# Kernel tuning notes

Hardware: AMD Instinct MI355X
Metric: run time of the kernel (lower is better)

## Reference

```python
import jax, jax.numpy as jnp
import numpy as np

Q_HEADS, KV_HEADS, DIMS = 16, 4, 1024
HEAD_DIM = DIMS // Q_HEADS          # 64
GROUPS = Q_HEADS // KV_HEADS        # 4
ROPE_BASE = 10000.0


def rope(x):
    # x: (..., s, d) -- standard interleaved rotary embedding, base 10000
    s, d = x.shape[-2], x.shape[-1]
    inv_freq = 1.0 / (ROPE_BASE ** (jnp.arange(0, d, 2, dtype=jnp.float32) / d))
    ang = jnp.arange(s, dtype=jnp.float32)[:, None] * inv_freq[None, :]  # (s, d/2)
    cos, sin = jnp.cos(ang), jnp.sin(ang)
    x1, x2 = x[..., 0::2], x[..., 1::2]
    out = jnp.stack([x1 * cos - x2 * sin, x1 * sin + x2 * cos], axis=-1)
    return out.reshape(x.shape).astype(x.dtype)


def setup_inputs() -> dict:
    key = jax.random.key(0)
    k1, k2, k3, k4, k5, k6 = jax.random.split(key, 6)
    B, S, E = 4, 2048, 1024
    q = jax.random.normal(k1, (B, S, E), dtype=jnp.float32)
    kv = jax.random.normal(k2, (B, S, E), dtype=jnp.float32)
    sc = 1.0 / np.sqrt(E)
    Wq = jax.random.normal(k3, (E, Q_HEADS, HEAD_DIM), dtype=jnp.float32) * sc
    Wk = jax.random.normal(k4, (E, KV_HEADS, HEAD_DIM), dtype=jnp.float32) * sc
    Wv = jax.random.normal(k5, (E, KV_HEADS, HEAD_DIM), dtype=jnp.float32) * sc
    Wo = jax.random.normal(k6, (HEAD_DIM, E), dtype=jnp.float32) / np.sqrt(HEAD_DIM)
    return {"q": q, "kv": kv, "Wq": Wq, "Wk": Wk, "Wv": Wv, "Wo": Wo}


def reference(q, kv, Wq, Wk, Wv, Wo):
    B, S, E = q.shape
    qh = jnp.einsum('bse,ehd->bshd', q, Wq)    # (B,S,Q_HEADS,hd)
    kh = jnp.einsum('bse,ehd->bshd', kv, Wk)   # (B,S,KV_HEADS,hd)
    vh = jnp.einsum('bse,ehd->bshd', kv, Wv)
    # rearrange '... s (h g) d -> ... g h s d' with g=GROUPS (h = KV_HEADS outer)
    qh = qh.reshape(B, S, KV_HEADS, GROUPS, HEAD_DIM).transpose(0, 3, 2, 1, 4)  # (B,g,h,S,d)
    kh = kh.transpose(0, 2, 1, 3)  # (B,h,S,d)
    vh = vh.transpose(0, 2, 1, 3)  # (B,h,S,d)
    qh = rope(qh)
    kh = rope(kh)
    # NOTE: sums over group axis g (faithful to original einsum)
    scores = jnp.einsum('bghsd,bhad->bhsa', qh, kh)
    attn = jax.nn.softmax(scores / (HEAD_DIM ** 0.5), axis=-1)
    out = jnp.einsum('bhsa,bhad->bhsd', attn, vh)  # (B,h,S,d)
    out = out.mean(axis=1)                          # mean over kv heads -> (B,S,d)
    return out @ Wo                                 # (B,S,E)
```

## Files before the change

kernel.cpp:

```cpp
#include <hip/hip_runtime.h>
#include <math.h>

#define SS 2048
#define EE 1024

using bf16x8 = __attribute__((ext_vector_type(8))) short;
using f32x4  = __attribute__((ext_vector_type(4))) float;

__device__ inline short f2bf(float x) {
    unsigned u = __builtin_bit_cast(unsigned, x);
    return (short)((u + 0x7fffu + ((u >> 16) & 1u)) >> 16);
}

__global__ __launch_bounds__(256) void prep_weights(const float* __restrict__ Wq,
                                                    const float* __restrict__ Wk,
                                                    const float* __restrict__ Wv,
                                                    const float* __restrict__ Wo,
                                                    short* __restrict__ Wall,
                                                    short* __restrict__ Wo4) {
    int idx = blockIdx.x * 256 + threadIdx.x;
    int c = idx >> 10, e = idx & 1023;
    int h = c >> 6, d = c & 63;
    const float* p = Wq + (size_t)e * 1024 + h * 256 + d;
    Wall[(size_t)c * 1024 + e] = f2bf(0.18033688011112042f * (p[0] + p[64] + p[128] + p[192]));
    Wall[(size_t)(256 + c) * 1024 + e] = f2bf(Wk[(size_t)e * 256 + c]);
    Wall[(size_t)(512 + c) * 1024 + e] = f2bf(Wv[(size_t)e * 256 + c]);
    Wo4[(size_t)e * 256 + c] = f2bf(0.25f * Wo[(size_t)d * 1024 + e]);
}

__global__ __launch_bounds__(256) void proj_kernel(const float* __restrict__ q,
                                                   const float* __restrict__ kv,
                                                   const short* __restrict__ Wall,
                                                   short* __restrict__ Qb,
                                                   short* __restrict__ Kb,
                                                   short* __restrict__ Vb) {
    __shared__ short As[128][72];
    __shared__ short Bs[64][72];
    int tid = threadIdx.x;
    int wave = tid >> 6, lane = tid & 63, quad = lane >> 4, c16 = lane & 15;
    int wm = wave >> 1, wn = wave & 1;
    int m0 = blockIdx.x * 128, n0 = blockIdx.y * 64;
    const float* A = (n0 < 256) ? q : kv;

    f32x4 acc[4][2];
    #pragma unroll
    for (int i = 0; i < 4; i++)
        #pragma unroll
        for (int j = 0; j < 2; j++) acc[i][j] = (f32x4){0.f, 0.f, 0.f, 0.f};

    for (int k0 = 0; k0 < 1024; k0 += 64) {
        #pragma unroll
        for (int i = 0; i < 8; i++) {
            int id = i * 256 + tid, r = id >> 4, ch = id & 15;
            float4 v = *(const float4*)&A[(size_t)(m0 + r) * 1024 + k0 + ch * 4];
            short4 s4;
            s4.x = f2bf(v.x); s4.y = f2bf(v.y); s4.z = f2bf(v.z); s4.w = f2bf(v.w);
            *(short4*)&As[r][ch * 4] = s4;
        }
        #pragma unroll
        for (int i = 0; i < 2; i++) {
            int id = i * 256 + tid, r = id >> 3, ch = id & 7;
            *(int4*)&Bs[r][ch * 8] =
                *(const int4*)&Wall[(size_t)(n0 + r) * 1024 + k0 + ch * 8];
        }
        __syncthreads();
        #pragma unroll
        for (int ks = 0; ks < 64; ks += 32) {
            bf16x8 af[4], bfr[2];
            #pragma unroll
            for (int mt = 0; mt < 4; mt++)
                af[mt] = *(const bf16x8*)&As[wm * 64 + mt * 16 + c16][ks + quad * 8];
            #pragma unroll
            for (int nt = 0; nt < 2; nt++)
                bfr[nt] = *(const bf16x8*)&Bs[wn * 32 + nt * 16 + c16][ks + quad * 8];
            #pragma unroll
            for (int mt = 0; mt < 4; mt++)
                #pragma unroll
                for (int nt = 0; nt < 2; nt++)
                    acc[mt][nt] = __builtin_amdgcn_mfma_f32_16x16x32_bf16(
                        af[mt], bfr[nt], acc[mt][nt], 0, 0, 0);
        }
        __syncthreads();
    }
    #pragma unroll
    for (int mt = 0; mt < 4; mt++) {
        #pragma unroll
        for (int nt = 0; nt < 2; nt++) {
            int col = n0 + wn * 32 + nt * 16 + c16;
            int rowb = m0 + wm * 64 + mt * 16 + quad * 4;
            f32x4 v = acc[mt][nt];
            short* dst = (col < 256) ? (Qb + col)
                       : (col < 512) ? (Kb + col - 256)
                                     : (Vb + col - 512);
            if (col < 512) {
                int d = col & 63, ii = d >> 1;
                float freq = __expf(-(float)ii * (9.210340371976184f / 32.0f));
                float sgn = (lane & 1) ? 1.0f : -1.0f;
                #pragma unroll
                for (int r = 0; r < 4; r++) {
                    int row = rowb + r;
                    float ang = (float)(row & (SS - 1)) * freq;
                    float sn, cs;
                    sincosf(ang, &sn, &cs);
                    float other = __shfl_xor(v[r], 1);
                    dst[(size_t)row * 256] = f2bf(v[r] * cs + sgn * sn * other);
                }
            } else {
                #pragma unroll
                for (int r = 0; r < 4; r++)
                    dst[(size_t)(rowb + r) * 256] = f2bf(v[r]);
            }
        }
    }
}

__global__ __launch_bounds__(256) void transpose_v(const short* __restrict__ Vb,
                                                   short* __restrict__ Vt) {
    __shared__ short T[64][72];
    int t = threadIdx.x;
    int s0 = blockIdx.x * 64, h = blockIdx.y, b = blockIdx.z;
    #pragma unroll
    for (int i = 0; i < 2; i++) {
        int id = i * 256 + t, sl = id >> 3, ch = id & 7;
        *(int4*)&T[sl][ch * 8] =
            *(const int4*)&Vb[((size_t)(b * SS + s0 + sl)) * 256 + h * 64 + ch * 8];
    }
    __syncthreads();
    #pragma unroll
    for (int i = 0; i < 2; i++) {
        int id = i * 256 + t, d = id >> 3, ch = id & 7;
        bf16x8 o;
        #pragma unroll
        for (int j = 0; j < 8; j++) o[j] = T[ch * 8 + j][d];
        *(bf16x8*)&Vt[((size_t)((b * 4 + h) * 64 + d)) * SS + s0 + ch * 8] = o;
    }
}

__global__ __launch_bounds__(256) void attn_kernel(const short* __restrict__ Qb,
                                                   const short* __restrict__ Kb,
                                                   const short* __restrict__ Vt,
                                                   float* __restrict__ Opart,
                                                   float* __restrict__ Lpart) {
    __shared__ short Qs[64][72], Ks[64][72], Vs[64][72];
    __shared__ short Ps[4][16][72];
    int tid = threadIdx.x;
    int wave = tid >> 6, lane = tid & 63, quad = lane >> 4, c16 = lane & 15;
    int qt = blockIdx.x, bh = blockIdx.y, kc = blockIdx.z;
    int q0 = qt * 64;
    size_t qkbase = (size_t)(bh >> 2) * SS * 256 + (bh & 3) * 64;
    size_t vtbase = (size_t)(bh * 64) * SS;
    size_t pbase  = (size_t)(kc * 16 + bh) * SS;

    #pragma unroll
    for (int i = 0; i < 2; i++) {
        int id = i * 256 + tid, r = id >> 3, ch = id & 7;
        *(int4*)&Qs[r][ch * 8] = *(const int4*)&Qb[qkbase + (size_t)(q0 + r) * 256 + ch * 8];
    }
    __syncthreads();
    bf16x8 aq0 = *(const bf16x8*)&Qs[wave * 16 + c16][quad * 8];
    bf16x8 aq1 = *(const bf16x8*)&Qs[wave * 16 + c16][32 + quad * 8];

    float lsum[4] = {0.f, 0.f, 0.f, 0.f};
    f32x4 o[4];
    #pragma unroll
    for (int dt = 0; dt < 4; dt++) o[dt] = (f32x4){0.f, 0.f, 0.f, 0.f};

    for (int kt = 0; kt < 16; kt++) {
        int a0 = kc * 1024 + kt * 64;
        __syncthreads();
        #pragma unroll
        for (int i = 0; i < 2; i++) {
            int id = i * 256 + tid, r = id >> 3, ch = id & 7;
            *(int4*)&Ks[r][ch * 8] =
                *(const int4*)&Kb[qkbase + (size_t)(a0 + r) * 256 + ch * 8];
            *(int4*)&Vs[r][ch * 8] =
                *(const int4*)&Vt[vtbase + (size_t)r * SS + a0 + ch * 8];
        }
        __syncthreads();
        f32x4 sv[4];
        #pragma unroll
        for (int nt = 0; nt < 4; nt++) sv[nt] = (f32x4){0.f, 0.f, 0.f, 0.f};
        #pragma unroll
        for (int nt = 0; nt < 4; nt++) {
            bf16x8 bk0 = *(const bf16x8*)&Ks[nt * 16 + c16][quad * 8];
            bf16x8 bk1 = *(const bf16x8*)&Ks[nt * 16 + c16][32 + quad * 8];
            sv[nt] = __builtin_amdgcn_mfma_f32_16x16x32_bf16(aq0, bk0, sv[nt], 0, 0, 0);
            sv[nt] = __builtin_amdgcn_mfma_f32_16x16x32_bf16(aq1, bk1, sv[nt], 0, 0, 0);
        }
        #pragma unroll
        for (int nt = 0; nt < 4; nt++)
            #pragma unroll
            for (int r = 0; r < 4; r++) sv[nt][r] = __builtin_exp2f(sv[nt][r]);
        #pragma unroll
        for (int r = 0; r < 4; r++)
            lsum[r] += (sv[0][r] + sv[1][r]) + (sv[2][r] + sv[3][r]);
        #pragma unroll
        for (int nt = 0; nt < 4; nt++)
            #pragma unroll
            for (int r = 0; r < 4; r++)
                Ps[wave][quad * 4 + r][nt * 16 + c16] = f2bf(sv[nt][r]);
        #pragma unroll
        for (int ks = 0; ks < 64; ks += 32) {
            bf16x8 ap = *(const bf16x8*)&Ps[wave][c16][ks + quad * 8];
            #pragma unroll
            for (int dt = 0; dt < 4; dt++) {
                bf16x8 bv = *(const bf16x8*)&Vs[dt * 16 + c16][ks + quad * 8];
                o[dt] = __builtin_amdgcn_mfma_f32_16x16x32_bf16(ap, bv, o[dt], 0, 0, 0);
            }
        }
    }
    #pragma unroll
    for (int off = 1; off < 16; off <<= 1)
        #pragma unroll
        for (int r = 0; r < 4; r++) lsum[r] += __shfl_xor(lsum[r], off);
    #pragma unroll
    for (int dt = 0; dt < 4; dt++)
        #pragma unroll
        for (int r = 0; r < 4; r++) {
            int row = q0 + wave * 16 + quad * 4 + r;
            Opart[(pbase + row) * 64 + dt * 16 + c16] = o[dt][r];
        }
    if (c16 == 0)
        #pragma unroll
        for (int r = 0; r < 4; r++)
            Lpart[pbase + q0 + wave * 16 + quad * 4 + r] = lsum[r];
}

__global__ __launch_bounds__(256) void combine_kernel(const float* __restrict__ Opart,
                                                      const float* __restrict__ Lpart,
                                                      float* __restrict__ Ob) {
    int idx = blockIdx.x * 256 + threadIdx.x;
    int d = idx & 63, h = (idx >> 6) & 3, s = (idx >> 8) & 2047, b = idx >> 19;
    int bh = b * 4 + h;
    size_t p0 = ((size_t)bh * SS + s) * 64 + d;
    size_t p1 = ((size_t)(16 + bh) * SS + s) * 64 + d;
    float o = Opart[p0] + Opart[p1];
    float l = Lpart[(size_t)bh * SS + s] + Lpart[(size_t)(16 + bh) * SS + s];
    Ob[((size_t)(b * SS + s)) * 256 + h * 64 + d] = o / l;
}

__global__ __launch_bounds__(256) void outproj_kernel(const float* __restrict__ Ob,
                                                      const short* __restrict__ Wo4,
                                                      float* __restrict__ out) {
    __shared__ short As[128][72];
    __shared__ short Bs[128][72];
    int tid = threadIdx.x;
    int wave = tid >> 6, lane = tid & 63, quad = lane >> 4, c16 = lane & 15;
    int wm = wave >> 1, wn = wave & 1;
    int m0 = blockIdx.x * 128, n0 = blockIdx.y * 128;

    f32x4 acc[4][4];
    #pragma unroll
    for (int i = 0; i < 4; i++)
        #pragma unroll
        for (int j = 0; j < 4; j++) acc[i][j] = (f32x4){0.f, 0.f, 0.f, 0.f};

    for (int k0 = 0; k0 < 256; k0 += 64) {
        #pragma unroll
        for (int i = 0; i < 8; i++) {
            int id = i * 256 + tid, r = id >> 4, ch = id & 15;
            float4 v = *(const float4*)&Ob[(size_t)(m0 + r) * 256 + k0 + ch * 4];
            short4 s4;
            s4.x = f2bf(v.x); s4.y = f2bf(v.y); s4.z = f2bf(v.z); s4.w = f2bf(v.w);
            *(short4*)&As[r][ch * 4] = s4;
        }
        #pragma unroll
        for (int i = 0; i < 4; i++) {
            int id = i * 256 + tid, r = id >> 3, ch = id & 7;
            *(int4*)&Bs[r][ch * 8] =
                *(const int4*)&Wo4[(size_t)(n0 + r) * 256 + k0 + ch * 8];
        }
        __syncthreads();
        #pragma unroll
        for (int ks = 0; ks < 64; ks += 32) {
            bf16x8 af[4], bfr[4];
            #pragma unroll
            for (int mt = 0; mt < 4; mt++)
                af[mt] = *(const bf16x8*)&As[wm * 64 + mt * 16 + c16][ks + quad * 8];
            #pragma unroll
            for (int nt = 0; nt < 4; nt++)
                bfr[nt] = *(const bf16x8*)&Bs[wn * 64 + nt * 16 + c16][ks + quad * 8];
            #pragma unroll
            for (int mt = 0; mt < 4; mt++)
                #pragma unroll
                for (int nt = 0; nt < 4; nt++)
                    acc[mt][nt] = __builtin_amdgcn_mfma_f32_16x16x32_bf16(
                        af[mt], bfr[nt], acc[mt][nt], 0, 0, 0);
        }
        __syncthreads();
    }
    #pragma unroll
    for (int mt = 0; mt < 4; mt++)
        #pragma unroll
        for (int nt = 0; nt < 4; nt++) {
            int col = n0 + wn * 64 + nt * 16 + c16;
            int rowb = m0 + wm * 64 + mt * 16 + quad * 4;
            #pragma unroll
            for (int r = 0; r < 4; r++)
                out[(size_t)(rowb + r) * 1024 + col] = acc[mt][nt][r];
        }
}

extern "C" void kernel_launch(void* const* d_in, const int* in_sizes, int n_in,
                              void* d_out, int out_size, void* d_ws, size_t ws_size,
                              hipStream_t stream) {
    const float* q  = (const float*)d_in[0];
    const float* kv = (const float*)d_in[1];
    const float* Wq = (const float*)d_in[2];
    const float* Wk = (const float*)d_in[3];
    const float* Wv = (const float*)d_in[4];
    const float* Wo = (const float*)d_in[5];
    float* out = (float*)d_out;

    short* Qb    = (short*)d_ws;
    short* Kb    = Qb + 2097152;
    short* Vb    = Kb + 2097152;
    short* Vt    = Vb + 2097152;
    short* Wall  = Vt + 2097152;
    short* Wo4   = Wall + 786432;
    float* Ob    = (float*)(Wo4 + 262144);
    float* Opart = Ob + 2097152;
    float* Lpart = Opart + 4194304;

    prep_weights<<<1024, 256, 0, stream>>>(Wq, Wk, Wv, Wo, Wall, Wo4);

    proj_kernel<<<dim3(64, 12), 256, 0, stream>>>(q, kv, Wall, Qb, Kb, Vb);

    transpose_v<<<dim3(32, 4, 4), 256, 0, stream>>>(Vb, Vt);

    attn_kernel<<<dim3(32, 16, 2), 256, 0, stream>>>(Qb, Kb, Vt, Opart, Lpart);

    combine_kernel<<<8192, 256, 0, stream>>>(Opart, Lpart, Ob);

    outproj_kernel<<<dim3(64, 8), 256, 0, stream>>>(Ob, Wo4, out);
}
```

Measured before the change: 212.4 us.

## Fuse V transpose into projection and split-K combine into output projection

The projection epilogue now writes V directly in transposed layout, so the separate transpose kernel is removed. The combine of the two split-K partial results is folded into the output projection's A-tile load, which removes the Ob round trip and one launch. RoPE cos/sin values are precomputed into a table in prep_weights instead of calling sincosf per element. bf16 conversion switches to cheaper round-half-up packing with perm, which changes the rounding behaviour slightly.

```diff
diff --git a/kernel.cpp b/kernel.cpp
--- a/kernel.cpp
+++ b/kernel.cpp
@@ -10,6 +10,14 @@
 __device__ inline short f2bf(float x) {
     unsigned u = __builtin_bit_cast(unsigned, x);
     return (short)((u + 0x7fffu + ((u >> 16) & 1u)) >> 16);
+}
+__device__ inline short f2bf_r(float x) {
+    return (short)((__builtin_bit_cast(unsigned, x) + 0x8000u) >> 16);
+}
+__device__ inline unsigned pk_bf16(float a, float b) {
+    unsigned ua = __builtin_bit_cast(unsigned, a) + 0x8000u;
+    unsigned ub = __builtin_bit_cast(unsigned, b) + 0x8000u;
+    return __builtin_amdgcn_perm(ub, ua, 0x07060302u);
 }
 
 __global__ __launch_bounds__(256) void prep_weights(const float* __restrict__ Wq,
@@ -17,7 +25,8 @@
                                                     const float* __restrict__ Wv,
                                                     const float* __restrict__ Wo,
                                                     short* __restrict__ Wall,
-                                                    short* __restrict__ Wo4) {
+                                                    short* __restrict__ Wo4,
+                                                    float2* __restrict__ RT) {
     int idx = blockIdx.x * 256 + threadIdx.x;
     int c = idx >> 10, e = idx & 1023;
     int h = c >> 6, d = c & 63;
@@ -26,14 +35,22 @@
     Wall[(size_t)(256 + c) * 1024 + e] = f2bf(Wk[(size_t)e * 256 + c]);
     Wall[(size_t)(512 + c) * 1024 + e] = f2bf(Wv[(size_t)e * 256 + c]);
     Wo4[(size_t)e * 256 + c] = f2bf(0.25f * Wo[(size_t)d * 1024 + e]);
+    if (idx < 65536) {
+        int s = idx >> 5, ii = idx & 31;
+        float freq = __expf(-(float)ii * (9.210340371976184f / 32.0f));
+        float sn, cs;
+        sincosf((float)s * freq, &sn, &cs);
+        RT[idx] = (float2){cs, sn};
+    }
 }
 
 __global__ __launch_bounds__(256) void proj_kernel(const float* __restrict__ q,
                                                    const float* __restrict__ kv,
                                                    const short* __restrict__ Wall,
+                                                   const float2* __restrict__ RT,
                                                    short* __restrict__ Qb,
                                                    short* __restrict__ Kb,
-                                                   short* __restrict__ Vb) {
+                                                   short* __restrict__ Vt) {
     __shared__ short As[128][72];
     __shared__ short Bs[64][72];
     int tid = threadIdx.x;
@@ -53,9 +70,10 @@
         for (int i = 0; i < 8; i++) {
             int id = i * 256 + tid, r = id >> 4, ch = id & 15;
             float4 v = *(const float4*)&A[(size_t)(m0 + r) * 1024 + k0 + ch * 4];
-            short4 s4;
-            s4.x = f2bf(v.x); s4.y = f2bf(v.y); s4.z = f2bf(v.z); s4.w = f2bf(v.w);
-            *(short4*)&As[r][ch * 4] = s4;
+            uint2 u;
+            u.x = pk_bf16(v.x, v.y);
+            u.y = pk_bf16(v.z, v.w);
+            *(uint2*)&As[r][ch * 4] = u;
         }
         #pragma unroll
         for (int i = 0; i < 2; i++) {
@@ -89,50 +107,26 @@
             int col = n0 + wn * 32 + nt * 16 + c16;
             int rowb = m0 + wm * 64 + mt * 16 + quad * 4;
             f32x4 v = acc[mt][nt];
-            short* dst = (col < 256) ? (Qb + col)
-                       : (col < 512) ? (Kb + col - 256)
-                                     : (Vb + col - 512);
             if (col < 512) {
-                int d = col & 63, ii = d >> 1;
-                float freq = __expf(-(float)ii * (9.210340371976184f / 32.0f));
+                short* dst = (col < 256) ? (Qb + col) : (Kb + col - 256);
+                int ii = (col & 63) >> 1;
                 float sgn = (lane & 1) ? 1.0f : -1.0f;
                 #pragma unroll
                 for (int r = 0; r < 4; r++) {
                     int row = rowb + r;
-                    float ang = (float)(row & (SS - 1)) * freq;
-                    float sn, cs;
-                    sincosf(ang, &sn, &cs);
+                    float2 cs = RT[(row & (SS - 1)) * 32 + ii];
                     float other = __shfl_xor(v[r], 1);
-                    dst[(size_t)row * 256] = f2bf(v[r] * cs + sgn * sn * other);
+                    dst[(size_t)row * 256] = f2bf_r(v[r] * cs.x + sgn * cs.y * other);
                 }
             } else {
-                #pragma unroll
-                for (int r = 0; r < 4; r++)
-                    dst[(size_t)(rowb + r) * 256] = f2bf(v[r]);
+                int c = col - 512;
+                int b = rowb >> 11, s0 = rowb & (SS - 1);
+                uint2 u;
+                u.x = pk_bf16(v[0], v[1]);
+                u.y = pk_bf16(v[2], v[3]);
+                *(uint2*)&Vt[((size_t)(b * 256 + c)) * SS + s0] = u;
             }
         }
-    }
-}
-
-__global__ __launch_bounds__(256) void transpose_v(const short* __restrict__ Vb,
-                                                   short* __restrict__ Vt) {
-    __shared__ short T[64][72];
-    int t = threadIdx.x;
-    int s0 = blockIdx.x * 64, h = blockIdx.y, b = blockIdx.z;
-    #pragma unroll
-    for (int i = 0; i < 2; i++) {
-        int id = i * 256 + t, sl = id >> 3, ch = id & 7;
-        *(int4*)&T[sl][ch * 8] =
-            *(const int4*)&Vb[((size_t)(b * SS + s0 + sl)) * 256 + h * 64 + ch * 8];
-    }
-    __syncthreads();
-    #pragma unroll
-    for (int i = 0; i < 2; i++) {
-        int id = i * 256 + t, d = id >> 3, ch = id & 7;
-        bf16x8 o;
-        #pragma unroll
-        for (int j = 0; j < 8; j++) o[j] = T[ch * 8 + j][d];
-        *(bf16x8*)&Vt[((size_t)((b * 4 + h) * 64 + d)) * SS + s0 + ch * 8] = o;
     }
 }
 
@@ -198,7 +192,7 @@
         for (int nt = 0; nt < 4; nt++)
             #pragma unroll
             for (int r = 0; r < 4; r++)
-                Ps[wave][quad * 4 + r][nt * 16 + c16] = f2bf(sv[nt][r]);
+                Ps[wave][quad * 4 + r][nt * 16 + c16] = f2bf_r(sv[nt][r]);
         #pragma unroll
         for (int ks = 0; ks < 64; ks += 32) {
             bf16x8 ap = *(const bf16x8*)&Ps[wave][c16][ks + quad * 8];
@@ -226,20 +220,8 @@
             Lpart[pbase + q0 + wave * 16 + quad * 4 + r] = lsum[r];
 }
 
-__global__ __launch_bounds__(256) void combine_kernel(const float* __restrict__ Opart,
-                                                      const float* __restrict__ Lpart,
-                                                      float* __restrict__ Ob) {
-    int idx = blockIdx.x * 256 + threadIdx.x;
-    int d = idx & 63, h = (idx >> 6) & 3, s = (idx >> 8) & 2047, b = idx >> 19;
-    int bh = b * 4 + h;
-    size_t p0 = ((size_t)bh * SS + s) * 64 + d;
-    size_t p1 = ((size_t)(16 + bh) * SS + s) * 64 + d;
-    float o = Opart[p0] + Opart[p1];
-    float l = Lpart[(size_t)bh * SS + s] + Lpart[(size_t)(16 + bh) * SS + s];
-    Ob[((size_t)(b * SS + s)) * 256 + h * 64 + d] = o / l;
-}
-
-__global__ __launch_bounds__(256) void outproj_kernel(const float* __restrict__ Ob,
+__global__ __launch_bounds__(256) void outproj_kernel(const float* __restrict__ Op,
+                                                      const float* __restrict__ Lp,
                                                       const short* __restrict__ Wo4,
                                                       float* __restrict__ out) {
     __shared__ short As[128][72];
@@ -256,13 +238,21 @@
         for (int j = 0; j < 4; j++) acc[i][j] = (f32x4){0.f, 0.f, 0.f, 0.f};
 
     for (int k0 = 0; k0 < 256; k0 += 64) {
+        int h = k0 >> 6;
         #pragma unroll
         for (int i = 0; i < 8; i++) {
             int id = i * 256 + tid, r = id >> 4, ch = id & 15;
-            float4 v = *(const float4*)&Ob[(size_t)(m0 + r) * 256 + k0 + ch * 4];
-            short4 s4;
-            s4.x = f2bf(v.x); s4.y = f2bf(v.y); s4.z = f2bf(v.z); s4.w = f2bf(v.w);
-            *(short4*)&As[r][ch * 4] = s4;
+            int row = m0 + r, b = row >> 11, s = row & (SS - 1);
+            int bh = b * 4 + h;
+            size_t pidx = ((size_t)bh * SS + s) * 64 + ch * 4;
+            float4 a = *(const float4*)&Op[pidx];
+            float4 c = *(const float4*)&Op[pidx + (size_t)16 * SS * 64];
+            float l = Lp[(size_t)bh * SS + s] + Lp[(size_t)(16 + bh) * SS + s];
+            float rl = __builtin_amdgcn_rcpf(l);
+            uint2 u;
+            u.x = pk_bf16((a.x + c.x) * rl, (a.y + c.y) * rl);
+            u.y = pk_bf16((a.z + c.z) * rl, (a.w + c.w) * rl);
+            *(uint2*)&As[r][ch * 4] = u;
         }
         #pragma unroll
         for (int i = 0; i < 4; i++) {
@@ -314,23 +304,18 @@
 
     short* Qb    = (short*)d_ws;
     short* Kb    = Qb + 2097152;
-    short* Vb    = Kb + 2097152;
-    short* Vt    = Vb + 2097152;
+    short* Vt    = Kb + 2097152;
     short* Wall  = Vt + 2097152;
     short* Wo4   = Wall + 786432;
-    float* Ob    = (float*)(Wo4 + 262144);
-    float* Opart = Ob + 2097152;
+    float2* RT   = (float2*)(Wo4 + 262144);
+    float* Opart = (float*)(RT + 65536);
     float* Lpart = Opart + 4194304;
 
-    prep_weights<<<1024, 256, 0, stream>>>(Wq, Wk, Wv, Wo, Wall, Wo4);
-
-    proj_kernel<<<dim3(64, 12), 256, 0, stream>>>(q, kv, Wall, Qb, Kb, Vb);
-
-    transpose_v<<<dim3(32, 4, 4), 256, 0, stream>>>(Vb, Vt);
+    prep_weights<<<1024, 256, 0, stream>>>(Wq, Wk, Wv, Wo, Wall, Wo4, RT);
+
+    proj_kernel<<<dim3(64, 12), 256, 0, stream>>>(q, kv, Wall, RT, Qb, Kb, Vt);
 
     attn_kernel<<<dim3(32, 16, 2), 256, 0, stream>>>(Qb, Kb, Vt, Opart, Lpart);
 
-    combine_kernel<<<8192, 256, 0, stream>>>(Opart, Lpart, Ob);
-
-    outproj_kernel<<<dim3(64, 8), 256, 0, stream>>>(Ob, Wo4, out);
-}
+    outproj_kernel<<<dim3(64, 8), 256, 0, stream>>>(Opart, Lpart, Wo4, out);
+}
```

Measured after the change: 217.7 us. 1.02x slower.
